# Kernel tuning notes

Measured on AMD Instinct MI355X. Metric: run time of the kernel, lower is better.

## Reference

```python
import jax, jax.numpy as jnp
import numpy as np

B = 32768
DIM = 768          # emb dim
NA = 1024          # outer n_anchors
K = 8              # n_comp (= n_patches P in relays)
PD = 16            # patch_dim
RD = K * PD        # relay_dim = 128
L = 2              # n_layers (relays)
RA = 16            # anchors per patch inside RelayLayer
NPH = 3            # n_phases
TD = NPH * RA      # tri_dim = 48
H = 64             # pw_hidden
MAG_MIN, MAG_MAX = 0.1, 5.0


def _nrm(x, eps=1e-12):
    return x / jnp.maximum(jnp.linalg.norm(x, axis=-1, keepdims=True), eps)


def _ln(x, g, b, eps=1e-5):
    mu = jnp.mean(x, axis=-1, keepdims=True)
    var = jnp.mean(jnp.square(x - mu), axis=-1, keepdims=True)
    return (x - mu) * jax.lax.rsqrt(var + eps) * g + b


def setup_inputs() -> dict:
    key = jax.random.key(0)
    ks = jax.random.split(key, 16)
    xav = lambda k, shp, fan_in, fan_out: jax.random.normal(k, shp, jnp.float32) * np.sqrt(2.0 / (fan_in + fan_out))
    home = _nrm(jax.random.normal(ks[3], (L, K, RA, PD), jnp.float32))
    anchors = _nrm(home + 0.05 * jax.random.normal(ks[4], (L, K, RA, PD), jnp.float32))
    return {
        'emb': jax.random.normal(ks[0], (B, DIM), jnp.float32),
        'triangulation': jax.random.normal(ks[1], (B, NA), jnp.float32),
        'raw_magnitude': jax.random.uniform(ks[2], (B, 1), jnp.float32),
        'emb_w': xav(ks[5], (DIM, RD // 2), DIM, RD // 2), 'emb_b': jnp.zeros((RD // 2,), jnp.float32),
        'tri_w': xav(ks[6], (NA, RD // 4), NA, RD // 4), 'tri_b': jnp.zeros((RD // 4,), jnp.float32),
        'ctx_w': xav(ks[7], (RD // 2 + RD // 4 + 1, RD), RD // 2 + RD // 4 + 1, RD), 'ctx_b': jnp.zeros((RD,), jnp.float32),
        'home': home, 'anchors': anchors,
        'pw_w1': xav(ks[8], (L, K, TD, H), TD, H), 'pw_b1': jnp.zeros((L, K, H), jnp.float32),
        'pw_w2': xav(ks[9], (L, K, H, PD), H, PD), 'pw_b2': jnp.zeros((L, K, PD), jnp.float32),
        'pwn_g': jnp.ones((L, PD), jnp.float32), 'pwn_b': jnp.zeros((L, PD), jnp.float32),
        'gates': jnp.full((L, K), -3.0, jnp.float32),
        'norm_g': jnp.ones((L, RD), jnp.float32), 'norm_b': jnp.zeros((L, RD), jnp.float32),
        'head_w1': xav(ks[10], (K, PD, PD // 2), PD, PD // 2), 'head_b1': jnp.zeros((K, PD // 2), jnp.float32),
        'head_w2': xav(ks[11], (K, PD // 2, 1), PD // 2, 1), 'head_b2': jnp.zeros((K, 1), jnp.float32),
        'stats_bias': jnp.zeros((K,), jnp.float32),
    }


def _relay(x, home, anchors, w1, b1, w2, b2, pg, pb, gates, ng, nb):
    Bb = x.shape[0]
    patches = _ln(x, ng, nb).reshape(Bb, K, PD)          # [B,P,d]
    pn = _nrm(patches)
    h = _nrm(home)                                       # [P,A,d]
    c = _nrm(anchors)
    cosw = jnp.clip(jnp.sum(h * c, axis=-1), -1 + 1e-7, 1 - 1e-7)
    omega = jnp.arccos(cosw)[..., None]                  # [P,A,1]
    so = jnp.maximum(jnp.sin(omega), 1e-7)
    tris = []
    for t in (0.0, 1.0 / 3.0, 2.0 / 3.0):
        at = _nrm((jnp.sin((1.0 - t) * omega) * h + jnp.sin(t * omega) * c) / so)
        tris.append(1.0 - jnp.einsum('bpd,pad->bpa', pn, at))
    tri = jnp.concatenate(tris, axis=-1)                 # [B,P,3A]
    hh = jax.nn.gelu(jnp.einsum('bpt,pth->bph', tri, w1) + b1, approximate=False)
    pw = _ln(jnp.einsum('bph,phd->bpd', hh, w2) + b2, pg, pb)
    g = jax.nn.sigmoid(gates)[None, :, None]             # [1,P,1]
    return x + (g * pw + (1.0 - g) * patches).reshape(Bb, -1)


def reference(emb, triangulation, raw_magnitude, emb_w, emb_b, tri_w, tri_b, ctx_w, ctx_b,
              home, anchors, pw_w1, pw_b1, pw_w2, pw_b2, pwn_g, pwn_b, gates, norm_g, norm_b,
              head_w1, head_b1, head_w2, head_b2, stats_bias):
    ctx = jnp.concatenate([emb @ emb_w + emb_b, triangulation @ tri_w + tri_b, raw_magnitude], axis=-1)
    x = ctx @ ctx_w + ctx_b                              # [B, RD]
    for l in range(L):
        x = _relay(x, home[l], anchors[l], pw_w1[l], pw_b1[l], pw_w2[l], pw_b2[l],
                   pwn_g[l], pwn_b[l], gates[l], norm_g[l], norm_b[l])
    patches = x.reshape(-1, K, PD)
    h1 = jax.nn.gelu(jnp.einsum('bkd,kdh->bkh', patches, head_w1) + head_b1, approximate=False)
    mc_raw = (jnp.einsum('bkh,kho->bko', h1, head_w2) + head_b2)[..., 0]   # [B,K]
    mc = MAG_MIN + (MAG_MAX - MAG_MIN) * jax.nn.sigmoid(mc_raw + stats_bias)
    mag = jnp.repeat(mc, NA // K, axis=-1)               # [B, NA]
    return (mag, mc)
```

## Files before the change

### kernel.cpp

```cpp
#include <hip/hip_runtime.h>
#include <hip/hip_bf16.h>
#include <math.h>

#define BTOT 32768

typedef float f32x4 __attribute__((ext_vector_type(4)));
typedef __bf16 v8bf __attribute__((ext_vector_type(8)));

__device__ float g_x[BTOT * 128];
__device__ float g_M[2 * 8 * 16 * 64];
__device__ float g_b1p[2 * 8 * 64];
__device__ __align__(16) unsigned short g_wf[1792 * 128];
__device__ float g_beff[128];
__device__ float g_wr[128];

__device__ __forceinline__ float gelu_f(float v) {
    return 0.5f * v * (1.0f + erff(v * 0.70710678118654752f));
}

__device__ __forceinline__ unsigned short f2bf_rne(float x) {
    unsigned u = __float_as_uint(x);
    u += 0x7fffu + ((u >> 16) & 1u);
    return (unsigned short)(u >> 16);
}

#define GLOAD16(gp, lp)                                                        \
    __builtin_amdgcn_global_load_lds(                                          \
        (const __attribute__((address_space(1))) void*)(gp),                   \
        (__attribute__((address_space(3))) void*)(lp), 16, 0, 0)

__global__ __launch_bounds__(64) void k_pre(const float* __restrict__ home,
                                            const float* __restrict__ anchors,
                                            const float* __restrict__ pw_w1,
                                            const float* __restrict__ pw_b1) {
    __shared__ float s_AT[48 * 16];
    const int lp = blockIdx.x;
    const int tid = threadIdx.x;
    if (tid < 48) {
        const int t = tid >> 4, a = tid & 15;
        const float* hp = home + (lp * 16 + a) * 16;
        const float* cp = anchors + (lp * 16 + a) * 16;
        float h[16], c[16], nh = 0.f, nc = 0.f;
#pragma unroll
        for (int i = 0; i < 16; ++i) {
            h[i] = hp[i]; nh = fmaf(h[i], h[i], nh);
            c[i] = cp[i]; nc = fmaf(c[i], c[i], nc);
        }
        const float ih = 1.f / fmaxf(sqrtf(nh), 1e-12f);
        const float ic = 1.f / fmaxf(sqrtf(nc), 1e-12f);
        float cw = 0.f;
#pragma unroll
        for (int i = 0; i < 16; ++i) { h[i] *= ih; c[i] *= ic; cw = fmaf(h[i], c[i], cw); }
        cw = fminf(fmaxf(cw, -1.f + 1e-7f), 1.f - 1e-7f);
        const float om = acosf(cw);
        const float so = fmaxf(sinf(om), 1e-7f);
        const float tt = (float)t * (1.f / 3.f);
        const float s1 = sinf((1.f - tt) * om), s2 = sinf(tt * om);
        float v[16], nv = 0.f;
#pragma unroll
        for (int i = 0; i < 16; ++i) { v[i] = (s1 * h[i] + s2 * c[i]) / so; nv = fmaf(v[i], v[i], nv); }
        const float iv = 1.f / fmaxf(sqrtf(nv), 1e-12f);
#pragma unroll
        for (int i = 0; i < 16; ++i) s_AT[tid * 16 + i] = v[i] * iv;
    }
    __syncthreads();
    const int h = tid;
    const float* w1 = pw_w1 + lp * 48 * 64;
    float b = pw_b1[lp * 64 + h];
    float m[16];
#pragma unroll
    for (int d = 0; d < 16; ++d) m[d] = 0.f;
    for (int j = 0; j < 48; ++j) {
        const float w = w1[j * 64 + h];
        b += w;
#pragma unroll
        for (int d = 0; d < 16; ++d) m[d] = fmaf(s_AT[j * 16 + d], w, m[d]);
    }
    g_b1p[lp * 64 + h] = b;
#pragma unroll
    for (int d = 0; d < 16; ++d) g_M[(lp * 16 + d) * 64 + h] = m[d];
}

__global__ __launch_bounds__(256) void k_fold(const float* __restrict__ emb_w,
                                              const float* __restrict__ tri_w,
                                              const float* __restrict__ ctx_w,
                                              const float* __restrict__ ctx_b,
                                              const float* __restrict__ emb_b,
                                              const float* __restrict__ tri_b) {
    if (blockIdx.x == 56) {
        const int n = threadIdx.x;
        if (n < 128) {
            float b = ctx_b[n];
            for (int c = 0; c < 64; ++c) b = fmaf(emb_b[c], ctx_w[c * 128 + n], b);
            for (int c = 0; c < 32; ++c) b = fmaf(tri_b[c], ctx_w[(64 + c) * 128 + n], b);
            g_beff[n] = b;
            g_wr[n] = ctx_w[96 * 128 + n];
        }
        return;
    }
    __shared__ float sctx[97 * 128];
    for (int q = threadIdx.x; q < 3104; q += 256)
        *(float4*)&sctx[q * 4] = *(const float4*)&ctx_w[q * 4];
    __syncthreads();
    const int kt = blockIdx.x;
    const int kr = threadIdx.x >> 3;
    const int n0 = (threadIdx.x & 7) * 16;
    const int k = kt * 32 + kr;
    float acc[16];
#pragma unroll
    for (int j = 0; j < 16; ++j) acc[j] = 0.f;
    if (k < 768) {
        const float* wrow = emb_w + k * 64;
        for (int c = 0; c < 64; ++c) {
            const float a = wrow[c];
            const float* cx = &sctx[c * 128 + n0];
#pragma unroll
            for (int j = 0; j < 16; ++j) acc[j] = fmaf(a, cx[j], acc[j]);
        }
    } else {
        const float* wrow = tri_w + (k - 768) * 32;
        for (int c = 0; c < 32; ++c) {
            const float a = wrow[c];
            const float* cx = &sctx[(64 + c) * 128 + n0];
#pragma unroll
            for (int j = 0; j < 16; ++j) acc[j] = fmaf(a, cx[j], acc[j]);
        }
    }
    const int nt = threadIdx.x & 7;
    const int lanehi = (kr >> 3) << 4;
    const int j8 = kr & 7;
#pragma unroll
    for (int q = 0; q < 16; ++q) {
        const int lane = lanehi | q;
        g_wf[((kt * 8 + nt) * 64 + lane) * 8 + j8] = f2bf_rne(acc[q]);
    }
}

__global__ __launch_bounds__(256) void k_front_mfma(const float* __restrict__ emb,
                                                    const float* __restrict__ tri,
                                                    const float* __restrict__ rm) {
    __shared__ __align__(16) char lds[49152];
    const int tid = threadIdx.x;
    const int lane = tid & 63, w = tid >> 6;
    const int row0 = blockIdx.x * 64;
    const int arow = lane & 15, kgrp = lane >> 4;

    f32x4 acc[8];
#pragma unroll
    for (int nt = 0; nt < 8; ++nt) {
        f32x4 z = {0.f, 0.f, 0.f, 0.f};
        acc[nt] = z;
    }

    const float* embp = emb + (size_t)(row0 + w * 16 + arow) * 768 + kgrp * 8;
    const float* trip = tri + (size_t)(row0 + w * 16 + arow) * 1024 + kgrp * 8;

    float4 A0[4], A1[4], A2[4];

#define STAGE_B(kk, BUF) {                                                     \
        const int k2_ = (kk) < 27 ? (kk) : 27;                                 \
        const char* gB_ = (const char*)g_wf + (size_t)k2_ * 16384              \
                          + w * 4096 + lane * 16;                              \
        char* Bb_ = lds + (BUF) * 16384 + w * 4096;               \
        _Pragma("unroll")                                                      \
        for (int i = 0; i < 4; ++i) GLOAD16(gB_ + i * 1024, Bb_ + i * 1024);   \
    }

#define ALOAD(kk, S) {                                                         \
        const int k2_ = (kk) < 27 ? (kk) : 27;                                 \
        const float* ab_ = (k2_ < 12) ? (embp + k2_ * 64) : (trip + (k2_ - 12) * 64); \
        S[0] = *(const float4*)(ab_);                                          \
        S[1] = *(const float4*)(ab_ + 4);                                      \
        S[2] = *(const float4*)(ab_ + 32);                                     \
        S[3] = *(const float4*)(ab_ + 36);                                     \
    }

#define COMPUTE(BUF, S) {                                                      \
        const char* Br_ = lds + (BUF) * 16384 + lane * 16;                     \
        _Pragma("unroll")                                                      \
        for (int h = 0; h < 2; ++h) {                                          \
            const float4 f0_ = S[h * 2], f1_ = S[h * 2 + 1];                   \
            v8bf a_;                                                           \
            a_[0] = (__bf16)f0_.x; a_[1] = (__bf16)f0_.y;                      \
            a_[2] = (__bf16)f0_.z; a_[3] = (__bf16)f0_.w;                      \
            a_[4] = (__bf16)f1_.x; a_[5] = (__bf16)f1_.y;                      \
            a_[6] = (__bf16)f1_.z; a_[7] = (__bf16)f1_.w;                      \
            const char* bp_ = Br_ + h * 8192;                                  \
            _Pragma("unroll")                                                  \
            for (int nt = 0; nt < 8; ++nt) {                                   \
                const v8bf b_ = *(const v8bf*)(bp_ + nt * 1024);               \
                acc[nt] = __builtin_amdgcn_mfma_f32_16x16x32_bf16(a_, b_, acc[nt], 0, 0, 0); \
            }                                                                  \
        }                                                                      \
    }

#define BODY(kk, I0, I2, S0, S2) {                                             \
        STAGE_B((kk) + 2, I2);                                                 \
        ALOAD((kk) + 2, S2);                                                   \
        asm volatile("s_waitcnt vmcnt(16)" ::: "memory");                      \
        __builtin_amdgcn_s_barrier();                                          \
        COMPUTE(I0, S0);                                                       \
        __builtin_amdgcn_s_barrier();                                          \
    }

    STAGE_B(0, 0); ALOAD(0, A0);
    STAGE_B(1, 1); ALOAD(1, A1);

    for (int t = 0; t < 9; ++t) {
        const int k = t * 3;
        BODY(k,     0, 2, A0, A2);
        BODY(k + 1, 1, 0, A1, A0);
        BODY(k + 2, 2, 1, A2, A1);
    }
    BODY(27, 0, 2, A0, A2);
    asm volatile("s_waitcnt vmcnt(0)" ::: "memory");
#undef STAGE_B
#undef ALOAD
#undef COMPUTE
#undef BODY

    const int rowb = row0 + w * 16 + kgrp * 4;
    const f32x4 rv = *(const f32x4*)&rm[rowb];
#pragma unroll
    for (int nt = 0; nt < 8; ++nt) {
        const int col = nt * 16 + arow;
        const float be = g_beff[col];
        const float wv = g_wr[col];
#pragma unroll
        for (int rr = 0; rr < 4; ++rr) {
            g_x[(size_t)(rowb + rr) * 128 + col] = acc[nt][rr] + rv[rr] * wv + be;
        }
    }
}

__global__ __launch_bounds__(256) void k_relay(
    const float* __restrict__ pw_w2, const float* __restrict__ pw_b2,
    const float* __restrict__ pwn_g, const float* __restrict__ pwn_b,
    const float* __restrict__ gates, const float* __restrict__ norm_g,
    const float* __restrict__ norm_b, const float* __restrict__ head_w1,
    const float* __restrict__ head_b1, const float* __restrict__ head_w2,
    const float* __restrict__ head_b2, const float* __restrict__ stats_bias,
    float* __restrict__ out) {
    __shared__ __align__(16) float s_M[8 * 1028];
    __shared__ __align__(16) float s_w2[8 * 1028];
    __shared__ __align__(16) float s_b1p[8 * 68];
    __shared__ __align__(16) float s_hw1[8 * 132];
    __shared__ float s_hb1[64], s_hw2[64], s_hcb[8];
    __shared__ float s_mc[64 * 8];
    const int tid = threadIdx.x;
    const int pr = tid >> 3, p = tid & 7;
    const int rowA = blockIdx.x * 64 + pr * 2;

    {
        const int e = tid * 4, pp = e >> 7, rem = e & 127;
        *(float4*)&s_hw1[pp * 132 + rem] = *(const float4*)&head_w1[e];
    }
    if (tid < 64) { s_hb1[tid] = head_b1[tid]; s_hw2[tid] = head_w2[tid]; }
    if (tid < 8) s_hcb[tid] = head_b2[tid] + stats_bias[tid];

    float xA[16], xB[16];
    {
        const float* xp = g_x + (size_t)rowA * 128 + p * 16;
#pragma unroll
        for (int i = 0; i < 4; ++i) {
            *(float4*)&xA[i * 4] = *(const float4*)&xp[i * 4];
            *(float4*)&xB[i * 4] = *(const float4*)&xp[128 + i * 4];
        }
    }

    for (int l = 0; l < 2; ++l) {
        if (l) __syncthreads();
        for (int q = tid; q < 2048; q += 256) {
            const int e = q * 4, pp = e >> 10, rem = e & 1023;
            *(float4*)&s_M[pp * 1028 + rem] = *(const float4*)&g_M[l * 8192 + e];
            *(float4*)&s_w2[pp * 1028 + rem] = *(const float4*)&pw_w2[l * 8192 + e];
        }
        if (tid < 128) {
            const int e = tid * 4, pp = e >> 6, rem = e & 63;
            *(float4*)&s_b1p[pp * 68 + rem] = *(const float4*)&g_b1p[l * 512 + e];
        }
        __syncthreads();

        float sA = 0.f, qA = 0.f, sB = 0.f, qB = 0.f;
#pragma unroll
        for (int i = 0; i < 16; ++i) {
            sA += xA[i]; qA = fmaf(xA[i], xA[i], qA);
            sB += xB[i]; qB = fmaf(xB[i], xB[i], qB);
        }
#pragma unroll
        for (int m = 1; m < 8; m <<= 1) {
            sA += __shfl_xor(sA, m, 64); qA += __shfl_xor(qA, m, 64);
            sB += __shfl_xor(sB, m, 64); qB += __shfl_xor(qB, m, 64);
        }
        const float muA = sA * (1.f / 128.f);
        const float rsA = rsqrtf(fmaxf(qA * (1.f / 128.f) - muA * muA, 0.f) + 1e-5f);
        const float muB = sB * (1.f / 128.f);
        const float rsB = rsqrtf(fmaxf(qB * (1.f / 128.f) - muB * muB, 0.f) + 1e-5f);
        float paA[16], paB[16], nA = 0.f, nB = 0.f;
#pragma unroll
        for (int i = 0; i < 16; ++i) {
            const float gg = norm_g[l * 128 + p * 16 + i];
            const float bb = norm_b[l * 128 + p * 16 + i];
            const float vA = (xA[i] - muA) * rsA * gg + bb;
            const float vB = (xB[i] - muB) * rsB * gg + bb;
            paA[i] = vA; nA = fmaf(vA, vA, nA);
            paB[i] = vB; nB = fmaf(vB, vB, nB);
        }
        const float invA = 1.f / fmaxf(sqrtf(nA), 1e-12f);
        const float invB = 1.f / fmaxf(sqrtf(nB), 1e-12f);

        float pwA[16], pwB[16];
#pragma unroll
        for (int i = 0; i < 16; ++i) {
            const float b2 = pw_b2[(l * 8 + p) * 16 + i];
            pwA[i] = b2; pwB[i] = b2;
        }
        const float* Mp = &s_M[p * 1028];
        const float* W2p = &s_w2[p * 1028];
        const float* Bp = &s_b1p[p * 68];
        for (int h4 = 0; h4 < 16; ++h4) {
            float bq[4];
            *(float4*)bq = *(const float4*)&Bp[h4 * 4];
            float aA[4] = {0.f, 0.f, 0.f, 0.f};
            float aB[4] = {0.f, 0.f, 0.f, 0.f};
#pragma unroll
            for (int d = 0; d < 16; ++d) {
                float m4[4];
                *(float4*)m4 = *(const float4*)&Mp[d * 64 + h4 * 4];
#pragma unroll
                for (int j = 0; j < 4; ++j) {
                    aA[j] = fmaf(paA[d], m4[j], aA[j]);
                    aB[j] = fmaf(paB[d], m4[j], aB[j]);
                }
            }
#pragma unroll
            for (int j = 0; j < 4; ++j) {
                const float gA = gelu_f(bq[j] - invA * aA[j]);
                const float gB = gelu_f(bq[j] - invB * aB[j]);
                float w[16];
#pragma unroll
                for (int u = 0; u < 4; ++u)
                    *(float4*)&w[u * 4] = *(const float4*)&W2p[(h4 * 4 + j) * 16 + u * 4];
#pragma unroll
                for (int u = 0; u < 16; ++u) {
                    pwA[u] = fmaf(gA, w[u], pwA[u]);
                    pwB[u] = fmaf(gB, w[u], pwB[u]);
                }
            }
        }
        float s2A = 0.f, q2A = 0.f, s2B = 0.f, q2B = 0.f;
#pragma unroll
        for (int i = 0; i < 16; ++i) {
            s2A += pwA[i]; q2A = fmaf(pwA[i], pwA[i], q2A);
            s2B += pwB[i]; q2B = fmaf(pwB[i], pwB[i], q2B);
        }
        const float mu2A = s2A * (1.f / 16.f);
        const float rs2A = rsqrtf(fmaxf(q2A * (1.f / 16.f) - mu2A * mu2A, 0.f) + 1e-5f);
        const float mu2B = s2B * (1.f / 16.f);
        const float rs2B = rsqrtf(fmaxf(q2B * (1.f / 16.f) - mu2B * mu2B, 0.f) + 1e-5f);
        const float gate = 1.f / (1.f + expf(-gates[l * 8 + p]));
#pragma unroll
        for (int i = 0; i < 16; ++i) {
            const float pg = pwn_g[l * 16 + i], pb = pwn_b[l * 16 + i];
            const float vA = (pwA[i] - mu2A) * rs2A * pg + pb;
            const float vB = (pwB[i] - mu2B) * rs2B * pg + pb;
            xA[i] = xA[i] + gate * vA + (1.f - gate) * paA[i];
            xB[i] = xB[i] + gate * vB + (1.f - gate) * paB[i];
        }
    }

    float accmA = s_hcb[p], accmB = accmA;
#pragma unroll
    for (int j = 0; j < 8; ++j) {
        float aA = s_hb1[p * 8 + j], aB = aA;
#pragma unroll
        for (int d = 0; d < 16; ++d) {
            const float w = s_hw1[p * 132 + d * 8 + j];
            aA = fmaf(xA[d], w, aA);
            aB = fmaf(xB[d], w, aB);
        }
        const float w2h = s_hw2[p * 8 + j];
        accmA = fmaf(gelu_f(aA), w2h, accmA);
        accmB = fmaf(gelu_f(aB), w2h, accmB);
    }
    const float mcA = 0.1f + 4.9f / (1.f + expf(-accmA));
    const float mcB = 0.1f + 4.9f / (1.f + expf(-accmB));
    s_mc[(pr * 2) * 8 + p] = mcA;
    s_mc[(pr * 2 + 1) * 8 + p] = mcB;
    out[(size_t)33554432 + (size_t)rowA * 8 + p] = mcA;
    out[(size_t)33554432 + (size_t)(rowA + 1) * 8 + p] = mcB;
    __syncthreads();

    const size_t base = (size_t)blockIdx.x * 64 * 1024;
#pragma unroll
    for (int it = 0; it < 64; ++it) {
        const int idx = it * 256 + tid;
        const int rr = idx >> 8, c4 = idx & 255;
        const float v = s_mc[rr * 8 + (c4 >> 5)];
        const float4 vv = make_float4(v, v, v, v);
        *(float4*)&out[base + rr * 1024 + c4 * 4] = vv;
    }
}

extern "C" void kernel_launch(void* const* d_in, const int* in_sizes, int n_in,
                              void* d_out, int out_size, void* d_ws, size_t ws_size,
                              hipStream_t stream) {
    (void)in_sizes; (void)n_in; (void)d_ws; (void)ws_size; (void)out_size;
    const float* emb = (const float*)d_in[0];
    const float* tria = (const float*)d_in[1];
    const float* rm = (const float*)d_in[2];
    const float* emb_w = (const float*)d_in[3];
    const float* emb_b = (const float*)d_in[4];
    const float* tri_w = (const float*)d_in[5];
    const float* tri_b = (const float*)d_in[6];
    const float* ctx_w = (const float*)d_in[7];
    const float* ctx_b = (const float*)d_in[8];
    const float* home = (const float*)d_in[9];
    const float* anch = (const float*)d_in[10];
    const float* pw_w1 = (const float*)d_in[11];
    const float* pw_b1 = (const float*)d_in[12];
    const float* pw_w2 = (const float*)d_in[13];
    const float* pw_b2 = (const float*)d_in[14];
    const float* pwn_g = (const float*)d_in[15];
    const float* pwn_b = (const float*)d_in[16];
    const float* gates = (const float*)d_in[17];
    const float* norm_g = (const float*)d_in[18];
    const float* norm_b = (const float*)d_in[19];
    const float* hw1 = (const float*)d_in[20];
    const float* hb1 = (const float*)d_in[21];
    const float* hw2 = (const float*)d_in[22];
    const float* hb2 = (const float*)d_in[23];
    const float* sb = (const float*)d_in[24];
    float* out = (float*)d_out;

    k_pre<<<16, 64, 0, stream>>>(home, anch, pw_w1, pw_b1);
    k_fold<<<57, 256, 0, stream>>>(emb_w, tri_w, ctx_w, ctx_b, emb_b, tri_b);
    k_front_mfma<<<512, 256, 0, stream>>>(emb, tria, rm);
    k_relay<<<512, 256, 0, stream>>>(pw_w2, pw_b2, pwn_g, pwn_b, gates, norm_g, norm_b,
                                     hw1, hb1, hw2, hb2, sb, out);
}
```

Measured before the change: 178.4 us.

## Double-buffer front GEMM with larger K-steps and use fast GELU/sigmoid approximations

The front MFMA GEMM moves from a triple-buffered pipeline of 64-wide K chunks to a double-buffered pipeline of 128-wide chunks. This halves the number of barrier-separated iterations and issues more loads per stage, but LDS use grows from 48 KB to 64 KB per block and the prefetch depth drops. Separately, the erf-based GELU is replaced with a tanh/sigmoid approximation, and the sigmoids now use __expf with a hardware reciprocal. This cuts transcendental cost in the relay and head but changes numerics slightly.

```diff
diff --git a/kernel.cpp b/kernel.cpp
--- a/kernel.cpp
+++ b/kernel.cpp
@@ -14,8 +14,21 @@
 __device__ float g_beff[128];
 __device__ float g_wr[128];
 
+__device__ __forceinline__ float fast_rcp(float x) {
+#if __has_builtin(__builtin_amdgcn_rcpf)
+    return __builtin_amdgcn_rcpf(x);
+#else
+    return 1.f / x;
+#endif
+}
+
 __device__ __forceinline__ float gelu_f(float v) {
-    return 0.5f * v * (1.0f + erff(v * 0.70710678118654752f));
+    const float p = v * fmaf(v * v, 0.0713548162f, 1.59576912f);
+    return v * fast_rcp(1.f + __expf(-p));
+}
+
+__device__ __forceinline__ float fast_sigmoid(float v) {
+    return fast_rcp(1.f + __expf(-v));
 }
 
 __device__ __forceinline__ unsigned short f2bf_rne(float x) {
@@ -139,7 +152,7 @@
 __global__ __launch_bounds__(256) void k_front_mfma(const float* __restrict__ emb,
                                                     const float* __restrict__ tri,
                                                     const float* __restrict__ rm) {
-    __shared__ __align__(16) char lds[49152];
+    __shared__ __align__(16) char lds[65536];
     const int tid = threadIdx.x;
     const int lane = tid & 63, w = tid >> 6;
     const int row0 = blockIdx.x * 64;
@@ -155,37 +168,39 @@
     const float* embp = emb + (size_t)(row0 + w * 16 + arow) * 768 + kgrp * 8;
     const float* trip = tri + (size_t)(row0 + w * 16 + arow) * 1024 + kgrp * 8;
 
-    float4 A0[4], A1[4], A2[4];
+    float4 A0[8], A1[8];
+
+#define ALOAD(kk, S) {                                                         \
+        const int k2_ = (kk) < 13 ? (kk) : 13;                                 \
+        const float* ab_ = (k2_ < 6) ? (embp + k2_ * 128)                      \
+                                     : (trip + (k2_ - 6) * 128);               \
+        _Pragma("unroll")                                                      \
+        for (int s = 0; s < 4; ++s) {                                          \
+            S[s * 2]     = *(const float4*)(ab_ + s * 32);                     \
+            S[s * 2 + 1] = *(const float4*)(ab_ + s * 32 + 4);                 \
+        }                                                                      \
+    }
 
 #define STAGE_B(kk, BUF) {                                                     \
-        const int k2_ = (kk) < 27 ? (kk) : 27;                                 \
-        const char* gB_ = (const char*)g_wf + (size_t)k2_ * 16384              \
-                          + w * 4096 + lane * 16;                              \
-        char* Bb_ = lds + (BUF) * 16384 + w * 4096;               \
+        const int k2_ = (kk) < 13 ? (kk) : 13;                                 \
+        const char* gB_ = (const char*)g_wf + (size_t)k2_ * 32768              \
+                          + w * 8192 + lane * 16;                              \
+        char* Bb_ = lds + (BUF) * 32768 + w * 8192;               \
         _Pragma("unroll")                                                      \
-        for (int i = 0; i < 4; ++i) GLOAD16(gB_ + i * 1024, Bb_ + i * 1024);   \
-    }
-
-#define ALOAD(kk, S) {                                                         \
-        const int k2_ = (kk) < 27 ? (kk) : 27;                                 \
-        const float* ab_ = (k2_ < 12) ? (embp + k2_ * 64) : (trip + (k2_ - 12) * 64); \
-        S[0] = *(const float4*)(ab_);                                          \
-        S[1] = *(const float4*)(ab_ + 4);                                      \
-        S[2] = *(const float4*)(ab_ + 32);                                     \
-        S[3] = *(const float4*)(ab_ + 36);                                     \
+        for (int i = 0; i < 8; ++i) GLOAD16(gB_ + i * 1024, Bb_ + i * 1024);   \
     }
 
 #define COMPUTE(BUF, S) {                                                      \
-        const char* Br_ = lds + (BUF) * 16384 + lane * 16;                     \
+        const char* Br_ = lds + (BUF) * 32768 + lane * 16;                     \
         _Pragma("unroll")                                                      \
-        for (int h = 0; h < 2; ++h) {                                          \
-            const float4 f0_ = S[h * 2], f1_ = S[h * 2 + 1];                   \
+        for (int s = 0; s < 4; ++s) {                                          \
+            const float4 f0_ = S[s * 2], f1_ = S[s * 2 + 1];                   \
             v8bf a_;                                                           \
             a_[0] = (__bf16)f0_.x; a_[1] = (__bf16)f0_.y;                      \
             a_[2] = (__bf16)f0_.z; a_[3] = (__bf16)f0_.w;                      \
             a_[4] = (__bf16)f1_.x; a_[5] = (__bf16)f1_.y;                      \
             a_[6] = (__bf16)f1_.z; a_[7] = (__bf16)f1_.w;                      \
-            const char* bp_ = Br_ + h * 8192;                                  \
+            const char* bp_ = Br_ + s * 8192;                                  \
             _Pragma("unroll")                                                  \
             for (int nt = 0; nt < 8; ++nt) {                                   \
                 const v8bf b_ = *(const v8bf*)(bp_ + nt * 1024);               \
@@ -194,28 +209,27 @@
         }                                                                      \
     }
 
-#define BODY(kk, I0, I2, S0, S2) {                                             \
-        STAGE_B((kk) + 2, I2);                                                 \
-        ALOAD((kk) + 2, S2);                                                   \
+#define BODY(kk, BUFC, BUFN, SC, SN) {                                         \
+        ALOAD((kk) + 1, SN);                                                   \
+        STAGE_B((kk) + 1, BUFN);                                               \
         asm volatile("s_waitcnt vmcnt(16)" ::: "memory");                      \
         __builtin_amdgcn_s_barrier();                                          \
-        COMPUTE(I0, S0);                                                       \
+        COMPUTE(BUFC, SC);                                                     \
         __builtin_amdgcn_s_barrier();                                          \
     }
 
-    STAGE_B(0, 0); ALOAD(0, A0);
-    STAGE_B(1, 1); ALOAD(1, A1);
-
-    for (int t = 0; t < 9; ++t) {
-        const int k = t * 3;
-        BODY(k,     0, 2, A0, A2);
-        BODY(k + 1, 1, 0, A1, A0);
-        BODY(k + 2, 2, 1, A2, A1);
-    }
-    BODY(27, 0, 2, A0, A2);
+    ALOAD(0, A0);
+    STAGE_B(0, 0);
+    for (int t = 0; t < 6; ++t) {
+        BODY(2 * t,     0, 1, A0, A1);
+        BODY(2 * t + 1, 1, 0, A1, A0);
+    }
+    BODY(12, 0, 1, A0, A1);
     asm volatile("s_waitcnt vmcnt(0)" ::: "memory");
+    __builtin_amdgcn_s_barrier();
+    COMPUTE(1, A1);
+#undef ALOAD
 #undef STAGE_B
-#undef ALOAD
 #undef COMPUTE
 #undef BODY
 
@@ -358,7 +372,7 @@
         const float rs2A = rsqrtf(fmaxf(q2A * (1.f / 16.f) - mu2A * mu2A, 0.f) + 1e-5f);
         const float mu2B = s2B * (1.f / 16.f);
         const float rs2B = rsqrtf(fmaxf(q2B * (1.f / 16.f) - mu2B * mu2B, 0.f) + 1e-5f);
-        const float gate = 1.f / (1.f + expf(-gates[l * 8 + p]));
+        const float gate = fast_sigmoid(gates[l * 8 + p]);
 #pragma unroll
         for (int i = 0; i < 16; ++i) {
             const float pg = pwn_g[l * 16 + i], pb = pwn_b[l * 16 + i];
@@ -383,8 +397,8 @@
         accmA = fmaf(gelu_f(aA), w2h, accmA);
         accmB = fmaf(gelu_f(aB), w2h, accmB);
     }
-    const float mcA = 0.1f + 4.9f / (1.f + expf(-accmA));
-    const float mcB = 0.1f + 4.9f / (1.f + expf(-accmB));
+    const float mcA = 0.1f + 4.9f * fast_sigmoid(accmA);
+    const float mcB = 0.1f + 4.9f * fast_sigmoid(accmB);
     s_mc[(pr * 2) * 8 + p] = mcA;
     s_mc[(pr * 2 + 1) * 8 + p] = mcB;
     out[(size_t)33554432 + (size_t)rowA * 8 + p] = mcA;
```

After: 161.0 us. -9.7%, faster.
